# Performance work log

Hardware: AMD Instinct MI355X
Metric: run time of the kernel (lower is better)

Reference implementation:

```python
import jax, jax.numpy as jnp
import numpy as np

N = 40000   # nodes
E = 150000  # edges (before self-loops)
G = 128     # graphs in batch
V = 20000   # vocab
D = 512     # embedding/hidden dim
H = 4       # heads (layers 0,1)
C = 128     # per-head channels (H*C = D)


def setup_inputs() -> dict:
    key = jax.random.key(0)
    ks = jax.random.split(key, 64)
    n = lambda i, shp, s=0.05: jax.random.normal(ks[i], shp, dtype=jnp.float32) * s
    inp = {}
    inp['node_ids'] = jax.random.randint(ks[0], (N,), 0, V, dtype=jnp.int32)
    inp['edge_index'] = jax.random.randint(ks[1], (2, E), 0, N, dtype=jnp.int32)
    inp['batch'] = jnp.sort(jax.random.randint(ks[2], (N,), 0, G, dtype=jnp.int32))
    inp['emb'] = n(3, (V, D), 0.02)
    # GAT layer 0: D -> H x C, concat
    inp['W0'] = n(4, (D, H * C)); inp['as0'] = n(5, (H, C)); inp['ad0'] = n(6, (H, C)); inp['b0'] = n(7, (D,), 0.01)
    # GAT layer 1: D -> H x C, concat
    inp['W1'] = n(8, (D, H * C)); inp['as1'] = n(9, (H, C)); inp['ad1'] = n(10, (H, C)); inp['b1'] = n(11, (D,), 0.01)
    inp['W2'] = n(12, (D, D)); inp['as2'] = n(13, (1, D)); inp['ad2'] = n(14, (1, D)); inp['b2'] = n(15, (D,), 0.01)
    # danger head
    inp['dW1'] = n(16, (D, D)); inp['db1'] = n(17, (D,), 0.01)
    inp['dg1'] = 1.0 + n(18, (D,), 0.02); inp['dbt1'] = n(19, (D,), 0.02)
    inp['drm1'] = n(20, (D,), 0.02); inp['drv1'] = jax.random.uniform(ks[21], (D,)) + 0.5
    inp['dW2'] = n(22, (D, D // 2)); inp['db2'] = n(23, (D // 2,), 0.01)
    inp['dg2'] = 1.0 + n(24, (D // 2,), 0.02); inp['dbt2'] = n(25, (D // 2,), 0.02)
    inp['drm2'] = n(26, (D // 2,), 0.02); inp['drv2'] = jax.random.uniform(ks[27], (D // 2,)) + 0.5
    inp['dW3'] = n(28, (D // 2, 1)); inp['db3'] = n(29, (1,), 0.01)
    # synergy head
    inp['sW1'] = n(30, (D, D)); inp['sb1'] = n(31, (D,), 0.01)
    inp['sg1'] = 1.0 + n(32, (D,), 0.02); inp['sbt1'] = n(33, (D,), 0.02)
    inp['srm1'] = n(34, (D,), 0.02); inp['srv1'] = jax.random.uniform(ks[35], (D,)) + 0.5
    inp['sW2'] = n(36, (D, D // 2)); inp['sb2'] = n(37, (D // 2,), 0.01)
    inp['sg2'] = 1.0 + n(38, (D // 2,), 0.02); inp['sbt2'] = n(39, (D // 2,), 0.02)
    inp['srm2'] = n(40, (D // 2,), 0.02); inp['srv2'] = jax.random.uniform(ks[41], (D // 2,)) + 0.5
    inp['sW3'] = n(42, (D // 2, 1)); inp['sb3'] = n(43, (1,), 0.01)
    return inp


def _gat(x, W, a_src, a_dst, bias, src, dst, heads, ch, concat):
    # PyG GATConv (eval): linear, per-head additive attention, softmax over
    # incoming edges per destination node, scatter-add aggregate.
    n_nodes = x.shape[0]
    h = (x @ W).reshape(n_nodes, heads, ch)              # [N,H,C]
    e_s = jnp.sum(h * a_src, axis=-1)                    # [N,H]
    e_d = jnp.sum(h * a_dst, axis=-1)                    # [N,H]
    e = jax.nn.leaky_relu(e_s[src] + e_d[dst], 0.2)      # [E,H]
    m = jax.ops.segment_max(e, dst, num_segments=n_nodes)
    m = jnp.where(jnp.isfinite(m), m, 0.0)
    p = jnp.exp(e - m[dst])
    s = jax.ops.segment_sum(p, dst, num_segments=n_nodes)
    alpha = p / (s[dst] + 1e-16)                         # [E,H]
    out = jax.ops.segment_sum(h[src] * alpha[:, :, None], dst, num_segments=n_nodes)
    out = out.reshape(n_nodes, heads * ch) if concat else out.mean(axis=1)
    return out + bias


def _bn(x, g, b, rm, rv):
    return (x - rm) * jax.lax.rsqrt(rv + 1e-5) * g + b


def _head(p, W1, b1, g1, bt1, rm1, rv1, W2, b2, g2, bt2, rm2, rv2, W3, b3):
    z = jax.nn.relu(_bn(p @ W1 + b1, g1, bt1, rm1, rv1))
    z = jax.nn.relu(_bn(z @ W2 + b2, g2, bt2, rm2, rv2))
    return jax.nn.sigmoid(z @ W3 + b3)


def reference(node_ids, edge_index, batch, emb, W0, as0, ad0, b0, W1, as1, ad1, b1, W2, as2, ad2, b2, dW1, db1, dg1, dbt1, drm1, drv1, dW2, db2, dg2, dbt2, drm2, drv2, dW3, db3, sW1, sb1, sg1, sbt1, srm1, srv1, sW2, sb2, sg2, sbt2, srm2, srv2, sW3, sb3):
    loops = jnp.arange(N, dtype=edge_index.dtype)
    src = jnp.concatenate([edge_index[0], loops])
    dst = jnp.concatenate([edge_index[1], loops])
    x = emb[node_ids]                                    # [N,D]
    # layer 0 (no residual)
    x = jax.nn.relu(_gat(x, W0, as0, ad0, b0, src, dst, H, C, True))
    # layer 1 (+residual)
    x = x + jax.nn.relu(_gat(x, W1, as1, ad1, b1, src, dst, H, C, True))
    # layer 2 (+residual)
    x = x + jax.nn.relu(_gat(x, W2, as2, ad2, b2, src, dst, 1, D, False))
    # global mean pool per graph
    sums = jax.ops.segment_sum(x, batch, num_segments=G)
    cnt = jax.ops.segment_sum(jnp.ones((N,), x.dtype), batch, num_segments=G)
    pooled = sums / jnp.maximum(cnt, 1.0)[:, None]       # [G,D]
    danger = _head(pooled, dW1, db1, dg1, dbt1, drm1, drv1, dW2, db2, dg2, dbt2, drm2, drv2, dW3, db3)
    synergy = _head(pooled, sW1, sb1, sg1, sbt1, srm1, srv1, sW2, sb2, sg2, sbt2, srm2, srv2, sW3, sb3)
    return danger, synergy
```

## Files before the change

### kernel.cpp

```cpp
#include <hip/hip_runtime.h>
#include <hip/hip_bf16.h>
#include <stdint.h>

#define NN 40000
#define EE 150000
#define ET 190000
#define GG 128
#define DD 512
#define VV 20000
#define VP 20480
#define MP 40064
#define WB 192
#define NPB0 10240
#define FB 743
#define CW 32
#define NB8 5000

typedef __hip_bfloat16 bf16;
typedef __attribute__((ext_vector_type(8))) short s16x8;
typedef __attribute__((ext_vector_type(4))) float f32v4;

__device__ __forceinline__ float b2f(bf16 v) { return __bfloat162float(v); }
__device__ __forceinline__ bf16  f2b(float v) { return __float2bfloat16(v); }
__device__ __forceinline__ unsigned f2bu(float v) {
    bf16 b = __float2bfloat16(v);
    return (unsigned)*(unsigned short*)&b;
}
__device__ __forceinline__ float lo16(unsigned u) { return __uint_as_float(u << 16); }
__device__ __forceinline__ float hi16(unsigned u) { return __uint_as_float(u & 0xffff0000u); }
__device__ __forceinline__ float s2f(short s) {
    return __uint_as_float(((unsigned)(unsigned short)s) << 16);
}

__device__ __forceinline__ void gl_lds16(const void* g, void* l) {
    __builtin_amdgcn_global_load_lds(
        (const __attribute__((address_space(1))) unsigned int*)g,
        (__attribute__((address_space(3))) unsigned int*)l, 16, 0, 0);
}

__global__ __launch_bounds__(256) void k_prep(const float* __restrict__ W0,
                                              const float* __restrict__ W1,
                                              const float* __restrict__ W2,
                                              bf16* __restrict__ Wt0,
                                              bf16* __restrict__ Wt1,
                                              bf16* __restrict__ Wt2,
                                              const float4* __restrict__ emb4,
                                              bf16* __restrict__ embb,
                                              const int* __restrict__ esrc,
                                              const int* __restrict__ edst,
                                              int* __restrict__ deg,
                                              int* __restrict__ csrf) {
    __shared__ float tile[64][65];
    int b = blockIdx.x, tid = threadIdx.x;
    if (b < WB) {
        int wi = b >> 6, tl = b & 63;
        const float* W; bf16* Wt;
        if (wi == 0)      { W = W0; Wt = Wt0; }
        else if (wi == 1) { W = W1; Wt = Wt1; }
        else              { W = W2; Wt = Wt2; }
        int n0 = (tl & 7) * 64, k0 = (tl >> 3) * 64;
        int rr = tid >> 4, cc = (tid & 15) * 4;
        #pragma unroll
        for (int i = 0; i < 4; i++) {
            int k = k0 + i * 16 + rr;
            float4 v = *(const float4*)(W + (size_t)k * DD + n0 + cc);
            tile[cc + 0][i * 16 + rr] = v.x;
            tile[cc + 1][i * 16 + rr] = v.y;
            tile[cc + 2][i * 16 + rr] = v.z;
            tile[cc + 3][i * 16 + rr] = v.w;
        }
        __syncthreads();
        #pragma unroll
        for (int i = 0; i < 4; i++) {
            int nl = i * 16 + rr;
            ushort4 o;
            o.x = (unsigned short)f2bu(tile[nl][cc + 0]);
            o.y = (unsigned short)f2bu(tile[nl][cc + 1]);
            o.z = (unsigned short)f2bu(tile[nl][cc + 2]);
            o.w = (unsigned short)f2bu(tile[nl][cc + 3]);
            *(ushort4*)(Wt + (size_t)(n0 + nl) * DD + k0 + cc) = o;
        }
    } else if (b < WB + NPB0) {
        int t = (b - WB) * 256 + tid;
        int v = t >> 7, c = t & 127;
        ushort4 u;
        if (v < VV) {
            float4 x = emb4[(size_t)v * 128 + c];
            u.x = (unsigned short)f2bu(x.x); u.y = (unsigned short)f2bu(x.y);
            u.z = (unsigned short)f2bu(x.z); u.w = (unsigned short)f2bu(x.w);
        } else { u.x = 0; u.y = 0; u.z = 0; u.w = 0; }
        *(ushort4*)(embb + (size_t)v * DD + c * 4) = u;
    } else {
        int e = (b - WB - NPB0) * 256 + tid;
        if (e >= ET) return;
        int dst, src;
        if (e < EE) { dst = edst[e]; src = esrc[e]; }
        else        { dst = e - EE;  src = dst; }
        int slot = atomicAdd(&deg[dst], 1);
        if (slot < CW) csrf[dst * CW + slot] = src;
    }
}

template <int H, int MT>
__global__ __launch_bounds__(512) void k_gemm_mfma(const bf16* __restrict__ A,
                                                   const bf16* __restrict__ Bt,
                                                   bf16* __restrict__ C,
                                                   const float* __restrict__ a_s,
                                                   const float* __restrict__ a_d,
                                                   float* __restrict__ es,
                                                   float* __restrict__ ed) {
    constexpr int K = DD, N = DD;
    constexpr int GNBFk = (MT / 8) * 32;
    __shared__ bf16 smem[4 * 128 * 64];
    bf16* lA0 = smem;
    bf16* lB0 = smem + 8192;
    bf16* lA1 = smem + 16384;
    bf16* lB1 = smem + 24576;
    int tid = threadIdx.x, lane = tid & 63, quad = lane >> 4, l16 = lane & 15;
    int w = tid >> 6;

    int bid = blockIdx.x, mt, nt;
    if (bid >= GNBFk) { int r = bid - GNBFk; mt = (MT & ~7) + (r >> 2); nt = r & 3; }
    else { nt = (bid & 31) >> 3; mt = (bid >> 5) * 8 + (bid & 7); }
    int m0 = mt * 128, n0 = nt * 128;
    int wm = (w & 1) * 64, wn = (w >> 1) * 32;

    int l8 = lane >> 3, c16 = (lane & 7) << 4;
    int scol = c16 ^ (l8 << 4);
    const char* pAg = (const char*)A + (size_t)(m0 + w * 16 + l8) * (K * 2) + scol;
    const char* pBg = (const char*)Bt + (size_t)(n0 + w * 16 + l8) * (K * 2) + scol;
    char* dA0 = (char*)lA0 + w * 2048;
    char* dB0 = (char*)lB0 + w * 2048;
    char* dA1 = (char*)lA1 + w * 2048;
    char* dB1 = (char*)lB1 + w * 2048;

    int aoff[2][4], boff[2][2];
    #pragma unroll
    for (int kk = 0; kk < 2; kk++) {
        #pragma unroll
        for (int i = 0; i < 4; i++) {
            int qb = (kk * 4 + quad) << 4;
            int rowA = wm + i * 16 + l16;
            aoff[kk][i] = rowA * 64 + ((qb ^ ((rowA & 7) << 4)) >> 1);
        }
        #pragma unroll
        for (int j = 0; j < 2; j++) {
            int qb = (kk * 4 + quad) << 4;
            int rowB = wn + j * 16 + l16;
            boff[kk][j] = rowB * 64 + ((qb ^ ((rowB & 7) << 4)) >> 1);
        }
    }

    f32v4 zero = 0;
    f32v4 acc[4][2];
    #pragma unroll
    for (int i = 0; i < 4; i++)
        #pragma unroll
        for (int j = 0; j < 2; j++) acc[i][j] = zero;

    auto stage = [&](int kb, char* dA, char* dB) {
        #pragma unroll
        for (int i = 0; i < 2; i++) {
            gl_lds16(pAg + i * 8192 + kb, dA + i * 1024);
            gl_lds16(pBg + i * 8192 + kb, dB + i * 1024);
        }
    };
    auto compute = [&](const bf16* bA, const bf16* bB) {
        #pragma unroll
        for (int kk = 0; kk < 2; kk++) {
            s16x8 a[4], b[2];
            #pragma unroll
            for (int i = 0; i < 4; i++) a[i] = *(const s16x8*)(bA + aoff[kk][i]);
            #pragma unroll
            for (int j = 0; j < 2; j++) b[j] = *(const s16x8*)(bB + boff[kk][j]);
            #pragma unroll
            for (int i = 0; i < 4; i++)
                #pragma unroll
                for (int j = 0; j < 2; j++)
                    acc[i][j] = __builtin_amdgcn_mfma_f32_16x16x32_bf16(a[i], b[j], acc[i][j], 0, 0, 0);
        }
    };

    stage(0, dA0, dB0);
    __syncthreads();
    #pragma unroll
    for (int k0 = 0; k0 < K; k0 += 128) {
        stage((k0 + 64) * 2, dA1, dB1);
        compute(lA0, lB0);
        __syncthreads();
        if (k0 + 128 < K) stage((k0 + 128) * 2, dA0, dB0);
        compute(lA1, lB1);
        __syncthreads();
    }

    float* asl = (float*)(smem + 8192);
    float* adl = asl + 128;
    if (tid < 128)       asl[tid] = a_s[n0 + tid];
    else if (tid < 256)  adl[tid - 128] = a_d[n0 + tid - 128];

    constexpr int ESTR = 136;
    bf16* ebuf = smem;
    int lrB = (w & 1) * 16 + quad * 4;
    int lr = tid >> 4, cc8 = (tid & 15) * 8;
    int grow = m0 + (lr >> 4) * 64 + (lr & 15);
    #pragma unroll
    for (int i = 0; i < 4; i++) {
        __syncthreads();
        #pragma unroll
        for (int j = 0; j < 2; j++) {
            int col = wn + j * 16 + l16;
            #pragma unroll
            for (int r = 0; r < 4; r++)
                ebuf[(lrB + r) * ESTR + col] = f2b(acc[i][j][r]);
        }
        __syncthreads();
        s16x8 v0 = *(s16x8*)(ebuf + lr * ESTR + cc8);
        float ses = 0.f, sed = 0.f;
        #pragma unroll
        for (int k = 0; k < 8; k++) {
            float x = s2f(v0[k]);
            ses += x * asl[cc8 + k];
            sed += x * adl[cc8 + k];
        }
        #pragma unroll
        for (int off = 1; off < 16; off <<= 1) {
            ses += __shfl_xor(ses, off, 64);
            sed += __shfl_xor(sed, off, 64);
        }
        int row = grow + i * 16;
        if ((tid & 15) == 0) {
            if (H == 4) {
                es[(size_t)row * 4 + nt] = ses;
                ed[(size_t)row * 4 + nt] = sed;
            } else {
                es[(size_t)nt * MP + row] = ses;
                ed[(size_t)nt * MP + row] = sed;
            }
        }
        *(s16x8*)(C + (size_t)row * N + n0 + cc8) = v0;
    }
}

template <int H, bool RES, bool FUSE, bool GI>
__global__ __launch_bounds__(256) void k_gat_aggregate(const bf16* __restrict__ h,
                                                       const float* __restrict__ es,
                                                       const float* __restrict__ ed,
                                                       const int* __restrict__ degv,
                                                       const int* __restrict__ csrf,
                                                       const float* __restrict__ bias,
                                                       bf16* __restrict__ xb,
                                                       const int* __restrict__ batch,
                                                       float* __restrict__ psum,
                                                       float* __restrict__ pp,
                                                       const int* __restrict__ idsmap) {
    __shared__ int   s_src[8][32];
    __shared__ float s_a[8][32 * H];
    __shared__ int   s_deg[8];
    __shared__ int   s_gb[FUSE ? 8 : 1];
    __shared__ int   s_g0;
    __shared__ float s_acc[FUSE ? 4 : 1][FUSE ? 8 : 1][FUSE ? 64 : 1];
    int tid = threadIdx.x, w = tid >> 6, lane = tid & 63;
    int half = lane >> 5, el = lane & 31;
    int nb = blockIdx.x * 8;
    if (FUSE && tid == 0) s_g0 = batch[nb];
    {
        int ln = w * 2 + half;
        int node = nb + ln;
        int deg = degv[node];
        if (deg > CW) deg = CW;
        if (el == 0) {
            s_deg[ln] = deg;
            if (FUSE) s_gb[ln] = batch[node];
        }
        float edl[H];
        if (H == 4) {
            int nd = GI ? idsmap[node] : node;
            #pragma unroll
            for (int hh = 0; hh < H; hh++) edl[hh] = ed[nd * H + hh];
        } else {
            edl[0] = ed[node] + ed[MP + node] + ed[2 * MP + node] + ed[3 * MP + node];
        }
        float e_h[H];
        #pragma unroll
        for (int hh = 0; hh < H; hh++) e_h[hh] = -1e30f;
        if (el < deg) {
            int src = csrf[node * CW + el];
            if (GI) src = idsmap[src];
            s_src[ln][el] = src;
            if (H == 4) {
                float4 e4 = *(const float4*)(es + (size_t)src * 4);
                float t4[4] = {e4.x, e4.y, e4.z, e4.w};
                #pragma unroll
                for (int hh = 0; hh < 4; hh++) {
                    float e = t4[hh] + edl[hh];
                    e_h[hh] = e > 0.f ? e : 0.2f * e;
                }
            } else {
                float esv = es[src] + es[MP + src] + es[2 * MP + src] + es[3 * MP + src];
                float e = esv + edl[0];
                e_h[0] = e > 0.f ? e : 0.2f * e;
            }
        }
        float m[H];
        #pragma unroll
        for (int hh = 0; hh < H; hh++) m[hh] = e_h[hh];
        #pragma unroll
        for (int off = 16; off; off >>= 1)
            #pragma unroll
            for (int hh = 0; hh < H; hh++) m[hh] = fmaxf(m[hh], __shfl_xor(m[hh], off, 64));
        float p[H], sum[H];
        #pragma unroll
        for (int hh = 0; hh < H; hh++) {
            p[hh] = (el < deg) ? __expf(e_h[hh] - m[hh]) : 0.f;
            sum[hh] = p[hh];
        }
        #pragma unroll
        for (int off = 16; off; off >>= 1)
            #pragma unroll
            for (int hh = 0; hh < H; hh++) sum[hh] += __shfl_xor(sum[hh], off, 64);
        if (el < deg)
            #pragma unroll
            for (int hh = 0; hh < H; hh++) s_a[ln][el * H + hh] = p[hh] / (sum[hh] + 1e-16f);
    }
    __syncthreads();

    int dbase = lane * 8;
    int hd = (H == 4) ? (lane >> 4) : 0;
    float4 bi0 = *(const float4*)(bias + dbase);
    float4 bi1 = *(const float4*)(bias + dbase + 4);
    int ln0 = w * 2, ln1 = w * 2 + 1;
    int deg0 = s_deg[ln0], deg1 = s_deg[ln1];
    int dmax = deg0 > deg1 ? deg0 : deg1;
    if (FUSE) {
        #pragma unroll
        for (int k = 0; k < 8; k++) s_acc[w][k][lane] = 0.f;
    }
    float A0[8] = {}, A1[8] = {};
    for (int i = 0; i < dmax; i++) {
        if (i < deg0) {
            uint4 u = *(const uint4*)(h + (size_t)s_src[ln0][i] * DD + dbase);
            float a = s_a[ln0][i * H + hd];
            A0[0] += a * lo16(u.x); A0[1] += a * hi16(u.x);
            A0[2] += a * lo16(u.y); A0[3] += a * hi16(u.y);
            A0[4] += a * lo16(u.z); A0[5] += a * hi16(u.z);
            A0[6] += a * lo16(u.w); A0[7] += a * hi16(u.w);
        }
        if (i < deg1) {
            uint4 u = *(const uint4*)(h + (size_t)s_src[ln1][i] * DD + dbase);
            float a = s_a[ln1][i * H + hd];
            A1[0] += a * lo16(u.x); A1[1] += a * hi16(u.x);
            A1[2] += a * lo16(u.y); A1[3] += a * hi16(u.y);
            A1[4] += a * lo16(u.z); A1[5] += a * hi16(u.z);
            A1[6] += a * lo16(u.w); A1[7] += a * hi16(u.w);
        }
    }
    #pragma unroll
    for (int t = 0; t < 2; t++) {
        float* A = (t == 0) ? A0 : A1;
        int nn = w * 2 + t;
        float v[8];
        v[0] = A[0] + bi0.x; v[1] = A[1] + bi0.y;
        v[2] = A[2] + bi0.z; v[3] = A[3] + bi0.w;
        v[4] = A[4] + bi1.x; v[5] = A[5] + bi1.y;
        v[6] = A[6] + bi1.z; v[7] = A[7] + bi1.w;
        #pragma unroll
        for (int k = 0; k < 8; k++) v[k] = fmaxf(v[k], 0.f);
        size_t base = (size_t)(nb + nn) * DD + dbase;
        if (RES) {
            uint4 u = *(const uint4*)(xb + base);
            v[0] += lo16(u.x); v[1] += hi16(u.x);
            v[2] += lo16(u.y); v[3] += hi16(u.y);
            v[4] += lo16(u.z); v[5] += hi16(u.z);
            v[6] += lo16(u.w); v[7] += hi16(u.w);
        }
        if (FUSE) {
            int gn = s_gb[nn];
            if (gn == s_g0) {
                #pragma unroll
                for (int k = 0; k < 8; k++) s_acc[w][k][lane] += v[k];
            } else {
                #pragma unroll
                for (int k = 0; k < 8; k++)
                    atomicAdd(&psum[(size_t)gn * DD + dbase + k], v[k]);
            }
        } else {
            uint4 o;
            o.x = f2bu(v[0]) | (f2bu(v[1]) << 16);
            o.y = f2bu(v[2]) | (f2bu(v[3]) << 16);
            o.z = f2bu(v[4]) | (f2bu(v[5]) << 16);
            o.w = f2bu(v[6]) | (f2bu(v[7]) << 16);
            *(uint4*)(xb + base) = o;
        }
    }
    if (FUSE) {
        __syncthreads();
        int d = tid << 1;
        float a0 = s_acc[0][d & 7][d >> 3] + s_acc[1][d & 7][d >> 3]
                 + s_acc[2][d & 7][d >> 3] + s_acc[3][d & 7][d >> 3];
        int d1 = d + 1;
        float a1 = s_acc[0][d1 & 7][d1 >> 3] + s_acc[1][d1 & 7][d1 >> 3]
                 + s_acc[2][d1 & 7][d1 >> 3] + s_acc[3][d1 & 7][d1 >> 3];
        float2 o = {a0, a1};
        *(float2*)(pp + (size_t)blockIdx.x * DD + d) = o;
    }
}

__global__ __launch_bounds__(256) void k_pool_red(const int* __restrict__ batch,
                                                  const float* __restrict__ pp,
                                                  float* __restrict__ psum) {
    int g = blockIdx.x;
    __shared__ int s_lo, s_hi;
    if (threadIdx.x == 0) {
        int lo = 0, hi = NB8;
        while (lo < hi) { int mid = (lo + hi) >> 1; if (batch[mid * 8] < g) lo = mid + 1; else hi = mid; }
        s_lo = lo;
        lo = 0; hi = NB8;
        while (lo < hi) { int mid = (lo + hi) >> 1; if (batch[mid * 8] < g + 1) lo = mid + 1; else hi = mid; }
        s_hi = lo;
    }
    __syncthreads();
    int d = threadIdx.x * 2;
    float a0 = 0.f, a1 = 0.f;
    for (int b = s_lo; b < s_hi; b++) {
        float2 v = *(const float2*)(pp + (size_t)b * DD + d);
        a0 += v.x; a1 += v.y;
    }
    psum[(size_t)g * DD + d]     += a0;
    psum[(size_t)g * DD + d + 1] += a1;
}

template <int Din, int Dout, bool FIRST>
__global__ __launch_bounds__(256) void k_head_batched(const float* __restrict__ inD,
                                                      const float* __restrict__ inS,
                                                      const int* __restrict__ batch,
                                                      const float* __restrict__ Wd, const float* __restrict__ bd,
                                                      const float* __restrict__ gd, const float* __restrict__ btd,
                                                      const float* __restrict__ rmd, const float* __restrict__ rvd,
                                                      const float* __restrict__ Ws, const float* __restrict__ bs_,
                                                      const float* __restrict__ gs, const float* __restrict__ bts,
                                                      const float* __restrict__ rms, const float* __restrict__ rvs,
                                                      float* __restrict__ outD,
                                                      float* __restrict__ outS) {
    const float *in, *W, *b, *ga, *bt, *rm, *rv; float* out;
    if (blockIdx.z == 0) { in = inD; W = Wd; b = bd; ga = gd; bt = btd; rm = rmd; rv = rvd; out = outD; }
    else                 { in = inS; W = Ws; b = bs_; ga = gs; bt = bts; rm = rms; rv = rvs; out = outS; }
    int tid = threadIdx.x;
    int j0 = blockIdx.x * 64;
    int g0 = blockIdx.y * 32;
    int g  = tid >> 3;
    int jj = (tid & 7) * 8;

    __shared__ float sW[128][64];
    __shared__ float sIn[32][129];
    __shared__ float s_inv[32];

    if (FIRST) {
        if (tid < 32) {
            int gg = g0 + tid;
            int lo = 0, hi = NN;
            while (lo < hi) { int mid = (lo + hi) >> 1; if (batch[mid] < gg) lo = mid + 1; else hi = mid; }
            int a = lo; lo = 0; hi = NN;
            while (lo < hi) { int mid = (lo + hi) >> 1; if (batch[mid] < gg + 1) lo = mid + 1; else hi = mid; }
            s_inv[tid] = 1.f / fmaxf((float)(lo - a), 1.f);
        }
        __syncthreads();
    }

    float acc[8] = {};
    for (int kc = 0; kc < Din; kc += 128) {
        __syncthreads();
        int jl = tid & 63, kq = (tid >> 6) * 32;
        #pragma unroll
        for (int r = 0; r < 32; r++)
            sW[kq + r][jl] = W[(size_t)(kc + kq + r) * Dout + j0 + jl];
        #pragma unroll
        for (int s = 0; s < 16; s++) {
            int idx = s * 256 + tid;
            int gl = idx >> 7, kl = idx & 127;
            float v = in[(size_t)(g0 + gl) * Din + kc + kl];
            if (FIRST) v *= s_inv[gl];
            sIn[gl][kl] = v;
        }
        __syncthreads();
        #pragma unroll 4
        for (int k = 0; k < 128; k++) {
            float s = sIn[g][k];
            f32v4 w0 = *(f32v4*)&sW[k][jj];
            f32v4 w1 = *(f32v4*)&sW[k][jj + 4];
            acc[0] += s * w0[0]; acc[1] += s * w0[1];
            acc[2] += s * w0[2]; acc[3] += s * w0[3];
            acc[4] += s * w1[0]; acc[5] += s * w1[1];
            acc[6] += s * w1[2]; acc[7] += s * w1[3];
        }
    }
    int gg = g0 + g;
    #pragma unroll
    for (int t = 0; t < 8; t++) {
        int j = j0 + jj + t;
        float sv = acc[t] + b[j];
        sv = (sv - rm[j]) * rsqrtf(rv[j] + 1e-5f) * ga[j] + bt[j];
        out[(size_t)gg * Dout + j] = sv > 0.f ? sv : 0.f;
    }
}

__global__ __launch_bounds__(64) void k_head_final2(const float* __restrict__ zD,
                                                    const float* __restrict__ zS,
                                                    const float* __restrict__ W3d, const float* __restrict__ b3d,
                                                    const float* __restrict__ W3s, const float* __restrict__ b3s,
                                                    float* __restrict__ out, int Din) {
    const float* z; const float* W3; const float* b3; float* o;
    if (blockIdx.y == 0) { z = zD; W3 = W3d; b3 = b3d; o = out; }
    else                 { z = zS; W3 = W3s; b3 = b3s; o = out + GG; }
    int g = blockIdx.x, lane = threadIdx.x;
    float s = 0.f;
    for (int k = lane; k < Din; k += 64) s += z[(size_t)g * Din + k] * W3[k];
    #pragma unroll
    for (int off = 32; off; off >>= 1) s += __shfl_xor(s, off, 64);
    if (lane == 0) {
        s += b3[0];
        o[g] = 1.f / (1.f + __expf(-s));
    }
}

extern "C" void kernel_launch(void* const* d_in, const int* in_sizes, int n_in,
                              void* d_out, int out_size, void* d_ws, size_t ws_size,
                              hipStream_t stream) {
    const int*   node_ids = (const int*)d_in[0];
    const int*   ei       = (const int*)d_in[1];
    const int*   batch    = (const int*)d_in[2];
    const float* emb      = (const float*)d_in[3];
    const float* W0  = (const float*)d_in[4],  *as0 = (const float*)d_in[5];
    const float* ad0 = (const float*)d_in[6],  *b0  = (const float*)d_in[7];
    const float* W1  = (const float*)d_in[8],  *as1 = (const float*)d_in[9];
    const float* ad1 = (const float*)d_in[10], *b1  = (const float*)d_in[11];
    const float* W2  = (const float*)d_in[12], *as2 = (const float*)d_in[13];
    const float* ad2 = (const float*)d_in[14], *b2  = (const float*)d_in[15];
    const float* dW1 = (const float*)d_in[16], *db1 = (const float*)d_in[17];
    const float* dg1 = (const float*)d_in[18], *dbt1= (const float*)d_in[19];
    const float* drm1= (const float*)d_in[20], *drv1= (const float*)d_in[21];
    const float* dW2 = (const float*)d_in[22], *db2 = (const float*)d_in[23];
    const float* dg2 = (const float*)d_in[24], *dbt2= (const float*)d_in[25];
    const float* drm2= (const float*)d_in[26], *drv2= (const float*)d_in[27];
    const float* dW3 = (const float*)d_in[28], *db3 = (const float*)d_in[29];
    const float* sW1 = (const float*)d_in[30], *sb1 = (const float*)d_in[31];
    const float* sg1 = (const float*)d_in[32], *sbt1= (const float*)d_in[33];
    const float* srm1= (const float*)d_in[34], *srv1= (const float*)d_in[35];
    const float* sW2 = (const float*)d_in[36], *sb2 = (const float*)d_in[37];
    const float* sg2 = (const float*)d_in[38], *sbt2= (const float*)d_in[39];
    const float* srm2= (const float*)d_in[40], *srv2= (const float*)d_in[41];
    const float* sW3 = (const float*)d_in[42], *sb3 = (const float*)d_in[43];

    const int* esrc = ei;
    const int* edst = ei + EE;

    char* p = (char*)d_ws;
    auto alloc = [&](size_t bytes) { char* r = p; p += (bytes + 255) & ~(size_t)255; return (void*)r; };
    bf16*  xb      = (bf16*)alloc((size_t)MP * DD * 2);
    bf16*  hbuf    = (bf16*)alloc((size_t)MP * DD * 2);
    bf16*  embb    = (bf16*)alloc((size_t)VP * DD * 2);
    bf16*  Wt0     = (bf16*)alloc((size_t)DD * DD * 2);
    bf16*  Wt1     = (bf16*)alloc((size_t)DD * DD * 2);
    bf16*  Wt2     = (bf16*)alloc((size_t)DD * DD * 2);
    float* esed    = (float*)alloc((size_t)6 * MP * 4 * 4);
    float* es0 = esed,              *ed0 = esed + (size_t)MP * 4;
    float* es1 = esed + (size_t)MP * 8,  *ed1 = esed + (size_t)MP * 12;
    float* es2 = esed + (size_t)MP * 16, *ed2 = esed + (size_t)MP * 20;
    int*   deg     = (int*)alloc((size_t)NN * 4);
    float* psum    = (float*)alloc((size_t)GG * DD * 4);
    int*   csrf    = (int*)alloc((size_t)NN * CW * 4);
    float* pp      = (float*)alloc((size_t)NB8 * DD * 4);
    float* z1d     = (float*)alloc((size_t)GG * DD * 4);
    float* z1s     = (float*)alloc((size_t)GG * DD * 4);
    float* z2d     = (float*)alloc((size_t)GG * 256 * 4);
    float* z2s     = (float*)alloc((size_t)GG * 256 * 4);

    hipMemsetAsync(deg, 0, (size_t)NN * 4 + (size_t)GG * DD * 4, stream);
    k_prep<<<WB + NPB0 + FB, 256, 0, stream>>>(W0, W1, W2, Wt0, Wt1, Wt2,
                                               (const float4*)emb, embb,
                                               esrc, edst, deg, csrf);

    k_gemm_mfma<4, VP / 128><<<(VP / 128) * 4, 512, 0, stream>>>(embb, Wt0, hbuf, as0, ad0, es0, ed0);
    k_gat_aggregate<4, false, false, true><<<NB8, 256, 0, stream>>>(hbuf, es0, ed0, deg, csrf, b0, xb, nullptr, nullptr, nullptr, node_ids);

    k_gemm_mfma<4, MP / 128><<<(MP / 128) * 4, 512, 0, stream>>>(xb, Wt1, hbuf, as1, ad1, es1, ed1);
    k_gat_aggregate<4, true, false, false><<<NB8, 256, 0, stream>>>(hbuf, es1, ed1, deg, csrf, b1, xb, nullptr, nullptr, nullptr, nullptr);

    k_gemm_mfma<1, MP / 128><<<(MP / 128) * 4, 512, 0, stream>>>(xb, Wt2, hbuf, as2, ad2, es2, ed2);
    k_gat_aggregate<1, true, true, false><<<NB8, 256, 0, stream>>>(hbuf, es2, ed2, deg, csrf, b2, xb, batch, psum, pp, nullptr);
    k_pool_red<<<GG, 256, 0, stream>>>(batch, pp, psum);

    float* outp = (float*)d_out;
    dim3 h1grid(DD / 64, GG / 32, 2);
    k_head_batched<DD, DD, true><<<h1grid, 256, 0, stream>>>(psum, psum, batch,
        dW1, db1, dg1, dbt1, drm1, drv1,
        sW1, sb1, sg1, sbt1, srm1, srv1, z1d, z1s);
    dim3 h2grid(256 / 64, GG / 32, 2);
    k_head_batched<DD, 256, false><<<h2grid, 256, 0, stream>>>(z1d, z1s, batch,
        dW2, db2, dg2, dbt2, drm2, drv2,
        sW2, sb2, sg2, sbt2, srm2, srv2, z2d, z2s);
    dim3 fgrid(GG, 2);
    k_head_final2<<<fgrid, 64, 0, stream>>>(z2d, z2s, dW3, db3, sW3, sb3, outp, 256);
}
```

Before: 444.8 us.

## Triple-buffer GEMM LDS staging with vmcnt waits and pre-map vocab ids in CSR

The MFMA GEMM moves from a double-buffered loop with two __syncthreads per iteration to a three-stage LDS ring. It waits with explicit s_waitcnt vmcnt and one barrier per k-step, so two future tiles are in flight while the current one is computed. Separately, the edge-build step now stores a second CSR array that already holds node_ids[src]. This removes the indirect id lookup from the layer-0 aggregation, at the cost of more LDS per block (lower occupancy) and an extra scattered write plus a gather in prep.

New measurement: 462.1 us. 1.04x slower.

```diff
diff --git a/kernel.cpp b/kernel.cpp
--- a/kernel.cpp
+++ b/kernel.cpp
@@ -20,6 +20,9 @@
 typedef __attribute__((ext_vector_type(8))) short s16x8;
 typedef __attribute__((ext_vector_type(4))) float f32v4;
 
+#define VMCNT4() asm volatile("s_waitcnt vmcnt(4)" ::: "memory")
+#define VMCNT0() asm volatile("s_waitcnt vmcnt(0)" ::: "memory")
+
 __device__ __forceinline__ float b2f(bf16 v) { return __bfloat162float(v); }
 __device__ __forceinline__ bf16  f2b(float v) { return __float2bfloat16(v); }
 __device__ __forceinline__ unsigned f2bu(float v) {
@@ -46,10 +49,12 @@
                                               bf16* __restrict__ Wt2,
                                               const float4* __restrict__ emb4,
                                               bf16* __restrict__ embb,
+                                              const int* __restrict__ ids,
                                               const int* __restrict__ esrc,
                                               const int* __restrict__ edst,
                                               int* __restrict__ deg,
-                                              int* __restrict__ csrf) {
+                                              int* __restrict__ csrf,
+                                              int* __restrict__ csrfv) {
     __shared__ float tile[64][65];
     int b = blockIdx.x, tid = threadIdx.x;
     if (b < WB) {
@@ -97,7 +102,10 @@
         if (e < EE) { dst = edst[e]; src = esrc[e]; }
         else        { dst = e - EE;  src = dst; }
         int slot = atomicAdd(&deg[dst], 1);
-        if (slot < CW) csrf[dst * CW + slot] = src;
+        if (slot < CW) {
+            csrf[dst * CW + slot]  = src;
+            csrfv[dst * CW + slot] = ids[src];
+        }
     }
 }
 
@@ -111,11 +119,8 @@
                                                    float* __restrict__ ed) {
     constexpr int K = DD, N = DD;
     constexpr int GNBFk = (MT / 8) * 32;
-    __shared__ bf16 smem[4 * 128 * 64];
-    bf16* lA0 = smem;
-    bf16* lB0 = smem + 8192;
-    bf16* lA1 = smem + 16384;
-    bf16* lB1 = smem + 24576;
+    __shared__ bf16 smem[49152];
+    char* sb = (char*)smem;
     int tid = threadIdx.x, lane = tid & 63, quad = lane >> 4, l16 = lane & 15;
     int w = tid >> 6;
 
@@ -129,10 +134,6 @@
     int scol = c16 ^ (l8 << 4);
     const char* pAg = (const char*)A + (size_t)(m0 + w * 16 + l8) * (K * 2) + scol;
     const char* pBg = (const char*)Bt + (size_t)(n0 + w * 16 + l8) * (K * 2) + scol;
-    char* dA0 = (char*)lA0 + w * 2048;
-    char* dB0 = (char*)lB0 + w * 2048;
-    char* dA1 = (char*)lA1 + w * 2048;
-    char* dB1 = (char*)lB1 + w * 2048;
 
     int aoff[2][4], boff[2][2];
     #pragma unroll
@@ -158,42 +159,47 @@
         #pragma unroll
         for (int j = 0; j < 2; j++) acc[i][j] = zero;
 
-    auto stage = [&](int kb, char* dA, char* dB) {
+    auto stage = [&](int t, int b) {
+        int kb = t * 128;
+        char* dA = sb + b * 32768 + w * 2048;
+        char* dB = sb + b * 32768 + 16384 + w * 2048;
         #pragma unroll
         for (int i = 0; i < 2; i++) {
             gl_lds16(pAg + i * 8192 + kb, dA + i * 1024);
             gl_lds16(pBg + i * 8192 + kb, dB + i * 1024);
         }
     };
-    auto compute = [&](const bf16* bA, const bf16* bB) {
+    auto compute = [&](int b) {
+        const bf16* bA = (const bf16*)(sb + b * 32768);
+        const bf16* bB = (const bf16*)(sb + b * 32768 + 16384);
         #pragma unroll
         for (int kk = 0; kk < 2; kk++) {
-            s16x8 a[4], b[2];
+            s16x8 a[4], bb[2];
             #pragma unroll
             for (int i = 0; i < 4; i++) a[i] = *(const s16x8*)(bA + aoff[kk][i]);
             #pragma unroll
-            for (int j = 0; j < 2; j++) b[j] = *(const s16x8*)(bB + boff[kk][j]);
+            for (int j = 0; j < 2; j++) bb[j] = *(const s16x8*)(bB + boff[kk][j]);
             #pragma unroll
             for (int i = 0; i < 4; i++)
                 #pragma unroll
                 for (int j = 0; j < 2; j++)
-                    acc[i][j] = __builtin_amdgcn_mfma_f32_16x16x32_bf16(a[i], b[j], acc[i][j], 0, 0, 0);
+                    acc[i][j] = __builtin_amdgcn_mfma_f32_16x16x32_bf16(a[i], bb[j], acc[i][j], 0, 0, 0);
         }
     };
 
-    stage(0, dA0, dB0);
+    stage(0, 0);
+    stage(1, 1);
+    #pragma unroll
+    for (int t = 0; t < 8; t++) {
+        if (t < 7) { VMCNT4(); } else { VMCNT0(); }
+        __builtin_amdgcn_s_barrier();
+        __builtin_amdgcn_sched_barrier(0);
+        if (t + 2 < 8) stage(t + 2, (t + 2) % 3);
+        compute(t % 3);
+    }
     __syncthreads();
-    #pragma unroll
-    for (int k0 = 0; k0 < K; k0 += 128) {
-        stage((k0 + 64) * 2, dA1, dB1);
-        compute(lA0, lB0);
-        __syncthreads();
-        if (k0 + 128 < K) stage((k0 + 128) * 2, dA0, dB0);
-        compute(lA1, lB1);
-        __syncthreads();
-    }
-
-    float* asl = (float*)(smem + 8192);
+
+    float* asl = (float*)(sb + 16384);
     float* adl = asl + 128;
     if (tid < 128)       asl[tid] = a_s[n0 + tid];
     else if (tid < 256)  adl[tid - 128] = a_d[n0 + tid - 128];
@@ -285,7 +291,6 @@
         for (int hh = 0; hh < H; hh++) e_h[hh] = -1e30f;
         if (el < deg) {
             int src = csrf[node * CW + el];
-            if (GI) src = idsmap[src];
             s_src[ln][el] = src;
             if (H == 4) {
                 float4 e4 = *(const float4*)(es + (size_t)src * 4);
@@ -568,6 +573,7 @@
     int*   deg     = (int*)alloc((size_t)NN * 4);
     float* psum    = (float*)alloc((size_t)GG * DD * 4);
     int*   csrf    = (int*)alloc((size_t)NN * CW * 4);
+    int*   csrfv   = (int*)alloc((size_t)NN * CW * 4);
     float* pp      = (float*)alloc((size_t)NB8 * DD * 4);
     float* z1d     = (float*)alloc((size_t)GG * DD * 4);
     float* z1s     = (float*)alloc((size_t)GG * DD * 4);
@@ -576,11 +582,11 @@
 
     hipMemsetAsync(deg, 0, (size_t)NN * 4 + (size_t)GG * DD * 4, stream);
     k_prep<<<WB + NPB0 + FB, 256, 0, stream>>>(W0, W1, W2, Wt0, Wt1, Wt2,
-                                               (const float4*)emb, embb,
-                                               esrc, edst, deg, csrf);
+                                               (const float4*)emb, embb, node_ids,
+                                               esrc, edst, deg, csrf, csrfv);
 
     k_gemm_mfma<4, VP / 128><<<(VP / 128) * 4, 512, 0, stream>>>(embb, Wt0, hbuf, as0, ad0, es0, ed0);
-    k_gat_aggregate<4, false, false, true><<<NB8, 256, 0, stream>>>(hbuf, es0, ed0, deg, csrf, b0, xb, nullptr, nullptr, nullptr, node_ids);
+    k_gat_aggregate<4, false, false, true><<<NB8, 256, 0, stream>>>(hbuf, es0, ed0, deg, csrfv, b0, xb, nullptr, nullptr, nullptr, node_ids);
 
     k_gemm_mfma<4, MP / 128><<<(MP / 128) * 4, 512, 0, stream>>>(xb, Wt1, hbuf, as1, ad1, es1, ed1);
     k_gat_aggregate<4, true, false, false><<<NB8, 256, 0, stream>>>(hbuf, es1, ed1, deg, csrf, b1, xb, nullptr, nullptr, nullptr, nullptr);
```
